# Kernel optimization log

Hardware: AMD Instinct MI355X
Metric: run time of the kernel (lower is better)

## Reference

```python
import jax, jax.numpy as jnp
import numpy as np

B, S, E, H = 2, 2048, 1024, 16
HD = E // H


def setup_inputs() -> dict:
    key = jax.random.key(0)
    ks = jax.random.split(key, 5)
    scale = 1.0 / np.sqrt(E)
    return {
        "x": jax.random.normal(ks[0], (B, S, E), dtype=jnp.float32),
        "Wq": jax.random.normal(ks[1], (H, HD, E), dtype=jnp.float32) * scale,
        "Wk": jax.random.normal(ks[2], (H, HD, E), dtype=jnp.float32) * scale,
        "Wv": jax.random.normal(ks[3], (H, HD, E), dtype=jnp.float32) * scale,
        "Wo": jax.random.normal(ks[4], (E, E), dtype=jnp.float32) * scale,
    }


def reference(x, Wq, Wk, Wv, Wo):
    # Batched per-head projections: torch Linear y = x @ W.T, W: [head_dim, E]
    q = jnp.einsum("bse,hde->bshd", x, Wq)  # [B,S,H,HD]
    k = jnp.einsum("bse,hde->bshd", x, Wk)
    v = jnp.einsum("bse,hde->bshd", x, Wv)
    # Scaled dot-product attention; original scales by sqrt(head_dim)
    scores = jnp.einsum("bqhd,bkhd->bhqk", q, k) / jnp.sqrt(jnp.float32(HD))
    attn = jax.nn.softmax(scores, axis=-1)  # [B,H,S,S]
    out_h = jnp.einsum("bhqk,bkhd->bqhd", attn, v)  # [B,S,H,HD]
    out_cat = out_h.reshape(x.shape[0], x.shape[1], -1)  # concat heads -> [B,S,E]
    return out_cat @ Wo.T
```

## Files before the change

kernel.cpp:

```cpp
#include <hip/hip_runtime.h>
#include <hip/hip_bf16.h>

typedef unsigned short u16;
typedef unsigned int u32;
typedef __attribute__((ext_vector_type(4))) float f32x4;
typedef __attribute__((ext_vector_type(16))) float f32x16;
typedef __attribute__((ext_vector_type(8))) short short8;
typedef __attribute__((ext_vector_type(8))) unsigned short u16x8;
typedef __attribute__((ext_vector_type(4))) unsigned short u16x4;
typedef __attribute__((ext_vector_type(4))) unsigned int u32x4;

#define BATCH 2
#define SEQ   2048
#define EMB   1024
#define NH    16
#define HD    64

__device__ inline u16 f2bf(float f) {
    unsigned u = __builtin_bit_cast(unsigned, f);
    unsigned r = u + 0x7FFFu + ((u >> 16) & 1u);
    return (u16)(r >> 16);
}

__device__ inline float fexp2(float x) {
    float r;
    asm("v_exp_f32 %0, %1" : "=v"(r) : "v"(x));
    return r;
}

__device__ inline void gload16(const void* g, void* l) {
    __builtin_amdgcn_global_load_lds(
        (const __attribute__((address_space(1))) unsigned int*)g,
        (__attribute__((address_space(3))) unsigned int*)l, 16, 0, 0);
}

__device__ inline short8 mk8(u32 a, u32 b, u32 c, u32 d) {
    u32x4 t; t[0] = a; t[1] = b; t[2] = c; t[3] = d;
    return __builtin_bit_cast(short8, t);
}

#define PACK_ST(st, w0,w1,w2,w3,w4,w5,w6,w7)                                   \
  {                                                                            \
    asm("v_cvt_pk_bf16_f32 %0, %1, %2" : "=v"(w0) : "v"(st[0]),  "v"(st[1]));  \
    asm("v_cvt_pk_bf16_f32 %0, %1, %2" : "=v"(w1) : "v"(st[2]),  "v"(st[3]));  \
    asm("v_cvt_pk_bf16_f32 %0, %1, %2" : "=v"(w2) : "v"(st[4]),  "v"(st[5]));  \
    asm("v_cvt_pk_bf16_f32 %0, %1, %2" : "=v"(w3) : "v"(st[6]),  "v"(st[7]));  \
    asm("v_permlane32_swap_b32 %0, %1" : "+v"(w0), "+v"(w2));                  \
    asm("v_permlane32_swap_b32 %0, %1" : "+v"(w1), "+v"(w3));                  \
    asm("v_cvt_pk_bf16_f32 %0, %1, %2" : "=v"(w4) : "v"(st[8]),  "v"(st[9]));  \
    asm("v_cvt_pk_bf16_f32 %0, %1, %2" : "=v"(w5) : "v"(st[10]), "v"(st[11])); \
    asm("v_cvt_pk_bf16_f32 %0, %1, %2" : "=v"(w6) : "v"(st[12]), "v"(st[13])); \
    asm("v_cvt_pk_bf16_f32 %0, %1, %2" : "=v"(w7) : "v"(st[14]), "v"(st[15])); \
    asm("v_permlane32_swap_b32 %0, %1" : "+v"(w4), "+v"(w6));                  \
    asm("v_permlane32_swap_b32 %0, %1" : "+v"(w5), "+v"(w7));                  \
  }

__global__ __launch_bounds__(256) void convert_all(
    const float* __restrict__ x,
    const float* __restrict__ Wq, const float* __restrict__ Wk, const float* __restrict__ Wv,
    u16* __restrict__ Xb, u16* __restrict__ Wqkv)
{
    const long gidx = (long)blockIdx.x * 2048 + (long)threadIdx.x * 8;
    const float* src;
    u16* dst;
    if (gidx < 4194304L) {
        src = x + gidx; dst = Xb + gidx;
    } else {
        const long r = gidx - 4194304L;
        const int w = (int)(r >> 20);
        const long off = r & 1048575L;
        src = (w == 0 ? Wq : w == 1 ? Wk : Wv) + off;
        dst = Wqkv + r;
    }
    f32x4 a = *(const f32x4*)src;
    f32x4 b = *(const f32x4*)(src + 4);
    u16x8 o;
    #pragma unroll
    for (int j = 0; j < 4; ++j) { o[j] = f2bf(a[j]); o[4 + j] = f2bf(b[j]); }
    *(u16x8*)dst = o;
}

__global__ __launch_bounds__(256) void convert_wo(
    const float* __restrict__ Wo, u16* __restrict__ Wob)
{
    const long gidx = (long)blockIdx.x * 2048 + (long)threadIdx.x * 8;
    f32x4 a = *(const f32x4*)(Wo + gidx);
    f32x4 b = *(const f32x4*)(Wo + gidx + 4);
    u16x8 o;
    #pragma unroll
    for (int j = 0; j < 4; ++j) { o[j] = f2bf(a[j]); o[4 + j] = f2bf(b[j]); }
    *(u16x8*)(Wob + gidx) = o;
}

__global__ __launch_bounds__(512, 2) void gemm256(
    const u16* __restrict__ A, const u16* __restrict__ Bb,
    u16* __restrict__ Qo, u16* __restrict__ Ko, u16* __restrict__ VTo)
{
    __shared__ u16 As[2][256 * 64];
    __shared__ u16 Bs[2][256 * 64];

    const int tid = threadIdx.x;
    const int lane = tid & 63;
    const int wid = tid >> 6;
    const int lr = lane & 15;
    const int lg = lane >> 4;
    const int wr = wid >> 2;
    const int wc = wid & 3;

    const int lin = blockIdx.y * 16 + blockIdx.x;
    const int swz = (lin & 7) * 24 + (lin >> 3);
    const int m0 = (swz & 15) * 256;
    const int n0 = (swz >> 4) * 256;

    const int grow = lane >> 3;
    const int schunk = ((lane & 7) ^ grow) << 4;

    auto issueTile = [&](int kt, int buf) {
        const int k0b = kt * 128;
        #pragma unroll
        for (int i = 0; i < 4; ++i) {
            const int row = i * 64 + wid * 8 + grow;
            gload16((const char*)A + (size_t)(m0 + row) * 2048 + k0b + schunk,
                    (char*)As[buf] + i * 8192 + wid * 1024);
            gload16((const char*)Bb + (size_t)(n0 + row) * 2048 + k0b + schunk,
                    (char*)Bs[buf] + i * 8192 + wid * 1024);
        }
    };

    issueTile(0, 0);
    issueTile(1, 1);

    f32x4 acc[8][4] = {};
    const int rsw = (lr & 7);

    for (int t = 0; t < 16; ++t) {
        if (t < 15) { asm volatile("s_waitcnt vmcnt(8)" ::: "memory"); }
        else        { asm volatile("s_waitcnt vmcnt(0)" ::: "memory"); }
        __builtin_amdgcn_sched_barrier(0);
        __builtin_amdgcn_s_barrier();
        __builtin_amdgcn_sched_barrier(0);

        const u16* Ac = As[t & 1];
        const u16* Bc = Bs[t & 1];

        short8 a[4][2], b0[2][2], b1[2][2];

        #pragma unroll
        for (int fi = 0; fi < 4; ++fi)
            #pragma unroll
            for (int ks = 0; ks < 2; ++ks)
                a[fi][ks] = *(const short8*)((const char*)Ac + (wr * 128 + fi * 16 + lr) * 128
                                             + (((ks * 4 + lg) ^ rsw) << 4));
        #pragma unroll
        for (int fj = 0; fj < 2; ++fj)
            #pragma unroll
            for (int ks = 0; ks < 2; ++ks)
                b0[fj][ks] = *(const short8*)((const char*)Bc + (wc * 64 + fj * 16 + lr) * 128
                                              + (((ks * 4 + lg) ^ rsw) << 4));
        __builtin_amdgcn_s_setprio(1);
        #pragma unroll
        for (int fi = 0; fi < 4; ++fi)
            #pragma unroll
            for (int fj = 0; fj < 2; ++fj)
                #pragma unroll
                for (int ks = 0; ks < 2; ++ks)
                    acc[fi][fj] = __builtin_amdgcn_mfma_f32_16x16x32_bf16(a[fi][ks], b0[fj][ks], acc[fi][fj], 0, 0, 0);
        __builtin_amdgcn_s_setprio(0);

        #pragma unroll
        for (int fj = 0; fj < 2; ++fj)
            #pragma unroll
            for (int ks = 0; ks < 2; ++ks)
                b1[fj][ks] = *(const short8*)((const char*)Bc + (wc * 64 + (fj + 2) * 16 + lr) * 128
                                              + (((ks * 4 + lg) ^ rsw) << 4));
        __builtin_amdgcn_s_setprio(1);
        #pragma unroll
        for (int fi = 0; fi < 4; ++fi)
            #pragma unroll
            for (int fj = 0; fj < 2; ++fj)
                #pragma unroll
                for (int ks = 0; ks < 2; ++ks)
                    acc[fi][fj + 2] = __builtin_amdgcn_mfma_f32_16x16x32_bf16(a[fi][ks], b1[fj][ks], acc[fi][fj + 2], 0, 0, 0);
        __builtin_amdgcn_s_setprio(0);

        #pragma unroll
        for (int fi = 0; fi < 4; ++fi)
            #pragma unroll
            for (int ks = 0; ks < 2; ++ks)
                a[fi][ks] = *(const short8*)((const char*)Ac + (wr * 128 + (fi + 4) * 16 + lr) * 128
                                             + (((ks * 4 + lg) ^ rsw) << 4));
        __builtin_amdgcn_s_setprio(1);
        #pragma unroll
        for (int fi = 0; fi < 4; ++fi)
            #pragma unroll
            for (int fj = 0; fj < 2; ++fj)
                #pragma unroll
                for (int ks = 0; ks < 2; ++ks)
                    acc[fi + 4][fj + 2] = __builtin_amdgcn_mfma_f32_16x16x32_bf16(a[fi][ks], b1[fj][ks], acc[fi + 4][fj + 2], 0, 0, 0);
        __builtin_amdgcn_s_setprio(0);

        __builtin_amdgcn_s_setprio(1);
        #pragma unroll
        for (int fi = 0; fi < 4; ++fi)
            #pragma unroll
            for (int fj = 0; fj < 2; ++fj)
                #pragma unroll
                for (int ks = 0; ks < 2; ++ks)
                    acc[fi + 4][fj] = __builtin_amdgcn_mfma_f32_16x16x32_bf16(a[fi][ks], b0[fj][ks], acc[fi + 4][fj], 0, 0, 0);
        __builtin_amdgcn_s_setprio(0);

        __builtin_amdgcn_sched_barrier(0);
        __builtin_amdgcn_s_barrier();
        __builtin_amdgcn_sched_barrier(0);
        if (t + 2 < 16) issueTile(t + 2, t & 1);
    }

    const int w = n0 >> 10;
    const float qs = (w == 0) ? 0.125f * 1.44269504f : 1.0f;
    const int mb = m0 + wr * 128;
    const int nb = n0 + wc * 64;
    #pragma unroll
    for (int fi = 0; fi < 8; ++fi) {
        #pragma unroll
        for (int fj = 0; fj < 4; ++fj) {
            const int m = mb + fi * 16 + lg * 4;
            const int nn = (nb + fj * 16 + lr) & 1023;
            const int h = nn >> 6, d = nn & 63;
            const int bb = m >> 11, s = m & 2047;
            const size_t bh = (size_t)(bb * NH + h);
            if (w == 2) {
                u16x4 v;
                #pragma unroll
                for (int i = 0; i < 4; ++i) v[i] = f2bf(acc[fi][fj][i]);
                *(u16x4*)&VTo[(bh * HD + d) * SEQ + s] = v;
            } else {
                u16* P = (w == 0) ? Qo : Ko;
                #pragma unroll
                for (int i = 0; i < 4; ++i)
                    P[(bh * SEQ + s + i) * HD + d] = f2bf(acc[fi][fj][i] * qs);
            }
        }
    }
}

__global__ __launch_bounds__(256) void gemm_out(
    const u16* __restrict__ A, const u16* __restrict__ Bb, float* __restrict__ Fo)
{
    __shared__ u16 As[2][128 * 64];
    __shared__ u16 Bs[2][128 * 64];

    const int tid = threadIdx.x;

    const int lin = blockIdx.y * 32 + blockIdx.x;
    const int swz = (lin & 7) * 32 + (lin >> 3);
    const int m0 = (swz & 31) * 128;
    const int n0 = (swz >> 5) * 128;

    const int lane = tid & 63;
    const int lr = lane & 15;
    const int lg = lane >> 4;
    const int wid = tid >> 6;
    const int wm = wid >> 1, wn = wid & 1;

    const int grow = lane >> 3;
    const int gcolb = ((lane & 7) ^ grow) << 4;
    const int rswz = (lr & 7);

    f32x4 acc[4][4] = {};

    auto issue = [&](int kt, int buf) {
        const int k0b = kt * 128;
        #pragma unroll
        for (int t = 0; t < 4; ++t) {
            const int row = (wid * 4 + t) * 8 + grow;
            gload16((const char*)A + (size_t)(m0 + row) * 2048 + k0b + gcolb,
                    (char*)As[buf] + (wid * 4 + t) * 1024);
            gload16((const char*)Bb + (size_t)(n0 + row) * 2048 + k0b + gcolb,
                    (char*)Bs[buf] + (wid * 4 + t) * 1024);
        }
    };

    issue(0, 0);
    issue(1, 1);

    for (int kt = 0; kt < 16; ++kt) {
        if (kt < 15) { asm volatile("s_waitcnt vmcnt(8)" ::: "memory"); }
        else         { asm volatile("s_waitcnt vmcnt(0)" ::: "memory"); }
        __builtin_amdgcn_sched_barrier(0);
        __builtin_amdgcn_s_barrier();
        __builtin_amdgcn_sched_barrier(0);

        const u16* Ac = As[kt & 1];
        const u16* Bc = Bs[kt & 1];
        #pragma unroll
        for (int kk = 0; kk < 2; ++kk) {
            short8 a[4], b[4];
            #pragma unroll
            for (int i = 0; i < 4; ++i)
                a[i] = *(const short8*)((const char*)Ac + (wm * 64 + i * 16 + lr) * 128
                                        + (((kk * 4 + lg) ^ rswz) << 4));
            #pragma unroll
            for (int i = 0; i < 4; ++i)
                b[i] = *(const short8*)((const char*)Bc + (wn * 64 + i * 16 + lr) * 128
                                        + (((kk * 4 + lg) ^ rswz) << 4));
            #pragma unroll
            for (int mi = 0; mi < 4; ++mi)
                #pragma unroll
                for (int ni = 0; ni < 4; ++ni)
                    acc[mi][ni] = __builtin_amdgcn_mfma_f32_16x16x32_bf16(a[mi], b[ni], acc[mi][ni], 0, 0, 0);
        }

        __builtin_amdgcn_sched_barrier(0);
        __builtin_amdgcn_s_barrier();
        __builtin_amdgcn_sched_barrier(0);
        if (kt + 2 < 16) issue(kt + 2, kt & 1);
    }

    const int mb = m0 + wm * 64;
    const int nb = n0 + wn * 64;
    #pragma unroll
    for (int mi = 0; mi < 4; ++mi)
        #pragma unroll
        for (int ni = 0; ni < 4; ++ni) {
            const int m = mb + mi * 16 + lg * 4;
            const int n = nb + ni * 16 + lr;
            #pragma unroll
            for (int i = 0; i < 4; ++i)
                Fo[(size_t)(m + i) * EMB + n] = acc[mi][ni][i];
        }
}

__global__ __launch_bounds__(256) void attn_fwd(
    const u16* __restrict__ Q, const u16* __restrict__ K,
    const u16* __restrict__ VT, u16* __restrict__ Cat)
{
    __shared__ u16 Ks[3][64 * 64];
    __shared__ u16 Vs[3][64 * 64];

    const int tid = threadIdx.x;
    const int lane = tid & 63;
    const int wid = tid >> 6;
    const int lq = lane & 31;
    const int hi = lane >> 5;

    const int lin = blockIdx.y * 16 + blockIdx.x;
    const int swz = (lin & 7) * 64 + (lin >> 3);
    const int qt = swz & 15;
    const int bh = swz >> 4;
    const int b = bh >> 4, h = bh & 15;

    const u16* Qg = Q + ((size_t)bh * SEQ + qt * 128 + wid * 32 + lq) * HD;
    short8 qf[4];
    #pragma unroll
    for (int ks = 0; ks < 4; ++ks)
        qf[ks] = *(const short8*)((const char*)Qg + ks * 32 + hi * 16);

    float lsum = 0.f;
    f32x16 ot0 = {}, ot1 = {};

    const u16* Kg = K + (size_t)bh * SEQ * HD;
    const u16* Vg = VT + (size_t)bh * HD * SEQ;

    const int srow = lane >> 3;
    const int schunk = ((lane & 7) ^ srow) << 4;

    auto issueKV = [&](int nt) {
        const int kv0 = nt * 64;
        const int slot = nt % 3;
        #pragma unroll
        for (int i = 0; i < 2; ++i) {
            const int krow = i * 32 + wid * 8 + srow;
            gload16((const char*)Kg + (size_t)(kv0 + krow) * 128 + schunk,
                    (char*)Ks[slot] + i * 4096 + wid * 1024);
            gload16((const char*)Vg + (size_t)krow * (SEQ * 2) + kv0 * 2 + schunk,
                    (char*)Vs[slot] + i * 4096 + wid * 1024);
        }
    };

    const int rsw = (lq & 7);

    auto tile = [&](const u16* Kbuf, const u16* Vbuf) {
        f32x16 st0 = {}, st1 = {};
        #pragma unroll
        for (int ks = 0; ks < 4; ++ks) {
            const int co = ((ks * 2 + hi) ^ rsw) << 4;
            const short8 kf0 = *(const short8*)((const char*)Kbuf + lq * 128 + co);
            const short8 kf1 = *(const short8*)((const char*)Kbuf + (32 + lq) * 128 + co);
            st0 = __builtin_amdgcn_mfma_f32_32x32x16_bf16(kf0, qf[ks], st0, 0, 0, 0);
            st1 = __builtin_amdgcn_mfma_f32_32x32x16_bf16(kf1, qf[ks], st1, 0, 0, 0);
        }

        #pragma unroll
        for (int i = 0; i < 16; ++i) {
            st0[i] = fexp2(st0[i]);
            st1[i] = fexp2(st1[i]);
        }
        float s0 = 0.f, s1 = 0.f, s2 = 0.f, s3 = 0.f;
        #pragma unroll
        for (int i = 0; i < 16; i += 4) {
            s0 += st0[i]     + st1[i];
            s1 += st0[i + 1] + st1[i + 1];
            s2 += st0[i + 2] + st1[i + 2];
            s3 += st0[i + 3] + st1[i + 3];
        }
        lsum += (s0 + s1) + (s2 + s3);

        u32 a0, a1, a2, a3, a4, a5, a6, a7;
        u32 c0, c1, c2, c3, c4, c5, c6, c7;
        PACK_ST(st0, a0, a1, a2, a3, a4, a5, a6, a7);
        PACK_ST(st1, c0, c1, c2, c3, c4, c5, c6, c7);
        const short8 pf0 = mk8(a0, a1, a2, a3);
        const short8 pf1 = mk8(a4, a5, a6, a7);
        const short8 pf2 = mk8(c0, c1, c2, c3);
        const short8 pf3 = mk8(c4, c5, c6, c7);

        #pragma unroll
        for (int ks = 0; ks < 4; ++ks) {
            const short8 pf = (ks == 0) ? pf0 : (ks == 1) ? pf1 : (ks == 2) ? pf2 : pf3;
            const int co = ((ks * 2 + hi) ^ rsw) << 4;
            const short8 vf0 = *(const short8*)((const char*)Vbuf + lq * 128 + co);
            const short8 vf1 = *(const short8*)((const char*)Vbuf + (32 + lq) * 128 + co);
            ot0 = __builtin_amdgcn_mfma_f32_32x32x16_bf16(vf0, pf, ot0, 0, 0, 0);
            ot1 = __builtin_amdgcn_mfma_f32_32x32x16_bf16(vf1, pf, ot1, 0, 0, 0);
        }
    };

    issueKV(0); issueKV(1); issueKV(2);

    for (int p = 0; p < 16; ++p) {
        if (p < 15) { asm volatile("s_waitcnt vmcnt(4)" ::: "memory"); }
        else        { asm volatile("s_waitcnt vmcnt(0)" ::: "memory"); }
        __builtin_amdgcn_sched_barrier(0);
        __builtin_amdgcn_s_barrier();
        __builtin_amdgcn_sched_barrier(0);

        const int s0 = (2 * p) % 3;
        const int s1 = (2 * p + 1) % 3;
        tile(Ks[s0], Vs[s0]);
        tile(Ks[s1], Vs[s1]);

        __builtin_amdgcn_sched_barrier(0);
        __builtin_amdgcn_s_barrier();
        __builtin_amdgcn_sched_barrier(0);
        const int t3 = 2 * p + 3;
        if (t3 < 32)     issueKV(t3);
        if (t3 + 1 < 32) issueKV(t3 + 1);
    }

    const float l = lsum + __shfl_xor(lsum, 32);
    const float invl = 1.f / l;
    const int qrow = qt * 128 + wid * 32 + lq;
    u16* ob = Cat + ((size_t)b * SEQ + qrow) * EMB + h * HD;
    #pragma unroll
    for (int g = 0; g < 4; ++g) {
        u16x4 o0, o1;
        #pragma unroll
        for (int i = 0; i < 4; ++i) {
            o0[i] = f2bf(ot0[g * 4 + i] * invl);
            o1[i] = f2bf(ot1[g * 4 + i] * invl);
        }
        *(u16x4*)&ob[g * 8 + hi * 4] = o0;
        *(u16x4*)&ob[32 + g * 8 + hi * 4] = o1;
    }
}

extern "C" void kernel_launch(void* const* d_in, const int* in_sizes, int n_in,
                              void* d_out, int out_size, void* d_ws, size_t ws_size,
                              hipStream_t stream) {
    const float* x  = (const float*)d_in[0];
    const float* Wq = (const float*)d_in[1];
    const float* Wk = (const float*)d_in[2];
    const float* Wv = (const float*)d_in[3];
    const float* Wo = (const float*)d_in[4];
    float* out = (float*)d_out;

    u16* Xb   = (u16*)d_out;
    u16* Wqkv = (u16*)d_out + (size_t)4 * 1048576;

    char* ws = (char*)d_ws;
    u16* Qb  = (u16*)(ws);
    u16* Kb  = (u16*)(ws + (size_t)8  * 1048576);
    u16* VTb = (u16*)(ws + (size_t)16 * 1048576);
    u16* Cat = (u16*)(ws + (size_t)24 * 1048576);
    u16* Wob = Qb;

    convert_all<<<3584, 256, 0, stream>>>(x, Wq, Wk, Wv, Xb, Wqkv);

    dim3 g1(4096 / 256, 3072 / 256);
    gemm256<<<g1, 512, 0, stream>>>(Xb, Wqkv, Qb, Kb, VTb);

    dim3 g2(SEQ / 128, BATCH * NH);
    attn_fwd<<<g2, 256, 0, stream>>>(Qb, Kb, VTb, Cat);

    convert_wo<<<512, 256, 0, stream>>>(Wo, Wob);
    dim3 g3(4096 / 128, 1024 / 128);
    gemm_out<<<g3, 256, 0, stream>>>(Cat, Wob, out);
}
```

Baseline: 124.3 us.

## Retile QKV GEMM to 256x192 blocks to fill all CUs

```diff
diff --git a/kernel.cpp b/kernel.cpp
--- a/kernel.cpp
+++ b/kernel.cpp
@@ -97,7 +97,7 @@
     u16* __restrict__ Qo, u16* __restrict__ Ko, u16* __restrict__ VTo)
 {
     __shared__ u16 As[2][256 * 64];
-    __shared__ u16 Bs[2][256 * 64];
+    __shared__ u16 Bs[2][192 * 64];
 
     const int tid = threadIdx.x;
     const int lane = tid & 63;
@@ -108,9 +108,9 @@
     const int wc = wid & 3;
 
     const int lin = blockIdx.y * 16 + blockIdx.x;
-    const int swz = (lin & 7) * 24 + (lin >> 3);
+    const int swz = (lin & 7) * 32 + (lin >> 3);
     const int m0 = (swz & 15) * 256;
-    const int n0 = (swz >> 4) * 256;
+    const int n0 = (swz >> 4) * 192;
 
     const int grow = lane >> 3;
     const int schunk = ((lane & 7) ^ grow) << 4;
@@ -122,6 +122,10 @@
             const int row = i * 64 + wid * 8 + grow;
             gload16((const char*)A + (size_t)(m0 + row) * 2048 + k0b + schunk,
                     (char*)As[buf] + i * 8192 + wid * 1024);
+        }
+        #pragma unroll
+        for (int i = 0; i < 3; ++i) {
+            const int row = i * 64 + wid * 8 + grow;
             gload16((const char*)Bb + (size_t)(n0 + row) * 2048 + k0b + schunk,
                     (char*)Bs[buf] + i * 8192 + wid * 1024);
         }
@@ -130,11 +134,11 @@
     issueTile(0, 0);
     issueTile(1, 1);
 
-    f32x4 acc[8][4] = {};
+    f32x4 acc[8][3] = {};
     const int rsw = (lr & 7);
 
     for (int t = 0; t < 16; ++t) {
-        if (t < 15) { asm volatile("s_waitcnt vmcnt(8)" ::: "memory"); }
+        if (t < 15) { asm volatile("s_waitcnt vmcnt(7)" ::: "memory"); }
         else        { asm volatile("s_waitcnt vmcnt(0)" ::: "memory"); }
         __builtin_amdgcn_sched_barrier(0);
         __builtin_amdgcn_s_barrier();
@@ -143,7 +147,7 @@
         const u16* Ac = As[t & 1];
         const u16* Bc = Bs[t & 1];
 
-        short8 a[4][2], b0[2][2], b1[2][2];
+        short8 a[4][2], b[3][2];
 
         #pragma unroll
         for (int fi = 0; fi < 4; ++fi)
@@ -152,35 +156,19 @@
                 a[fi][ks] = *(const short8*)((const char*)Ac + (wr * 128 + fi * 16 + lr) * 128
                                              + (((ks * 4 + lg) ^ rsw) << 4));
         #pragma unroll
-        for (int fj = 0; fj < 2; ++fj)
+        for (int fj = 0; fj < 3; ++fj)
             #pragma unroll
             for (int ks = 0; ks < 2; ++ks)
-                b0[fj][ks] = *(const short8*)((const char*)Bc + (wc * 64 + fj * 16 + lr) * 128
-                                              + (((ks * 4 + lg) ^ rsw) << 4));
+                b[fj][ks] = *(const short8*)((const char*)Bc + (wc * 48 + fj * 16 + lr) * 128
+                                             + (((ks * 4 + lg) ^ rsw) << 4));
         __builtin_amdgcn_s_setprio(1);
         #pragma unroll
         for (int fi = 0; fi < 4; ++fi)
             #pragma unroll
-            for (int fj = 0; fj < 2; ++fj)
+            for (int fj = 0; fj < 3; ++fj)
                 #pragma unroll
                 for (int ks = 0; ks < 2; ++ks)
-                    acc[fi][fj] = __builtin_amdgcn_mfma_f32_16x16x32_bf16(a[fi][ks], b0[fj][ks], acc[fi][fj], 0, 0, 0);
-        __builtin_amdgcn_s_setprio(0);
-
-        #pragma unroll
-        for (int fj = 0; fj < 2; ++fj)
-            #pragma unroll
-            for (int ks = 0; ks < 2; ++ks)
-                b1[fj][ks] = *(const short8*)((const char*)Bc + (wc * 64 + (fj + 2) * 16 + lr) * 128
-                                              + (((ks * 4 + lg) ^ rsw) << 4));
-        __builtin_amdgcn_s_setprio(1);
-        #pragma unroll
-        for (int fi = 0; fi < 4; ++fi)
-            #pragma unroll
-            for (int fj = 0; fj < 2; ++fj)
-                #pragma unroll
-                for (int ks = 0; ks < 2; ++ks)
-                    acc[fi][fj + 2] = __builtin_amdgcn_mfma_f32_16x16x32_bf16(a[fi][ks], b1[fj][ks], acc[fi][fj + 2], 0, 0, 0);
+                    acc[fi][fj] = __builtin_amdgcn_mfma_f32_16x16x32_bf16(a[fi][ks], b[fj][ks], acc[fi][fj], 0, 0, 0);
         __builtin_amdgcn_s_setprio(0);
 
         #pragma unroll
@@ -193,39 +181,30 @@
         #pragma unroll
         for (int fi = 0; fi < 4; ++fi)
             #pragma unroll
-            for (int fj = 0; fj < 2; ++fj)
+            for (int fj = 0; fj < 3; ++fj)
                 #pragma unroll
                 for (int ks = 0; ks < 2; ++ks)
-                    acc[fi + 4][fj + 2] = __builtin_amdgcn_mfma_f32_16x16x32_bf16(a[fi][ks], b1[fj][ks], acc[fi + 4][fj + 2], 0, 0, 0);
+                    acc[fi + 4][fj] = __builtin_amdgcn_mfma_f32_16x16x32_bf16(a[fi][ks], b[fj][ks], acc[fi + 4][fj], 0, 0, 0);
         __builtin_amdgcn_s_setprio(0);
 
-        __builtin_amdgcn_s_setprio(1);
-        #pragma unroll
-        for (int fi = 0; fi < 4; ++fi)
-            #pragma unroll
-            for (int fj = 0; fj < 2; ++fj)
-                #pragma unroll
-                for (int ks = 0; ks < 2; ++ks)
-                    acc[fi + 4][fj] = __builtin_amdgcn_mfma_f32_16x16x32_bf16(a[fi][ks], b0[fj][ks], acc[fi + 4][fj], 0, 0, 0);
-        __builtin_amdgcn_s_setprio(0);
-
         __builtin_amdgcn_sched_barrier(0);
         __builtin_amdgcn_s_barrier();
         __builtin_amdgcn_sched_barrier(0);
         if (t + 2 < 16) issueTile(t + 2, t & 1);
     }
 
-    const int w = n0 >> 10;
-    const float qs = (w == 0) ? 0.125f * 1.44269504f : 1.0f;
     const int mb = m0 + wr * 128;
-    const int nb = n0 + wc * 64;
-    #pragma unroll
-    for (int fi = 0; fi < 8; ++fi) {
-        #pragma unroll
-        for (int fj = 0; fj < 4; ++fj) {
+    const int nb = n0 + wc * 48;
+    #pragma unroll
+    for (int fj = 0; fj < 3; ++fj) {
+        const int nblk = nb + fj * 16;
+        const int w = nblk >> 10;
+        const float qs = (w == 0) ? 0.125f * 1.44269504f : 1.0f;
+        const int nn = (nblk & 1023) + lr;
+        const int h = nn >> 6, d = nn & 63;
+        #pragma unroll
+        for (int fi = 0; fi < 8; ++fi) {
             const int m = mb + fi * 16 + lg * 4;
-            const int nn = (nb + fj * 16 + lr) & 1023;
-            const int h = nn >> 6, d = nn & 63;
             const int bb = m >> 11, s = m & 2047;
             const size_t bh = (size_t)(bb * NH + h);
             if (w == 2) {
@@ -486,7 +465,7 @@
 
     convert_all<<<3584, 256, 0, stream>>>(x, Wq, Wk, Wv, Xb, Wqkv);
 
-    dim3 g1(4096 / 256, 3072 / 256);
+    dim3 g1(16, 16);
     gemm256<<<g1, 512, 0, stream>>>(Xb, Wqkv, Qb, Kb, VTb);
 
     dim3 g2(SEQ / 128, BATCH * NH);
```

Measured after the change: 119.4 us. 1.04x faster.
